# Optimization experiments

Hardware: AMD Instinct MI355X
Metric: run time of the kernel (lower is better)

## Reference

```python
import jax, jax.numpy as jnp
import numpy as np

DIM = 256
HEADS = 8
HD = DIM // HEADS        # head_dim = 32
WS = 8                   # window_size (Wh = Ww = 8)
NEXP = 8                 # num_experts
HID = 128                # attr_hidden_size (router hidden)
SCALE = HD ** -0.5


def _window_partition(x, ws):
    # (B, H, W, C) -> (B * H//ws * W//ws, ws, ws, C)
    B, H, W, C = x.shape
    x = x.reshape(B, H // ws, ws, W // ws, ws, C)
    return x.transpose(0, 1, 3, 2, 4, 5).reshape(-1, ws, ws, C)


def _window_reverse(w, ws, B, H, W):
    # inverse of _window_partition
    C = w.shape[-1]
    x = w.reshape(B, H // ws, W // ws, ws, ws, C)
    return x.transpose(0, 1, 3, 2, 4, 5).reshape(B, H, W, C)


def _rope2(x):
    # 2D rotary embedding over a window: x (B*, Wh, Ww, d).
    # First d/2 channels rotated by row position, last d/2 by column position.
    B, Wh, Ww, d = x.shape
    d2 = d // 2

    def angles(L, dd):
        inv = 1.0 / (10000.0 ** (jnp.arange(0, dd, 2, dtype=jnp.float32) / dd))
        return jnp.arange(L, dtype=jnp.float32)[:, None] * inv[None, :]  # (L, dd//2)

    def rotate(v, ang, bshape):
        # v: (B, Wh, Ww, dd) pairs interleaved; ang broadcast as bshape
        p = v.reshape(*v.shape[:-1], -1, 2)
        c = jnp.cos(ang).reshape(bshape)
        s = jnp.sin(ang).reshape(bshape)
        o0 = p[..., 0] * c - p[..., 1] * s
        o1 = p[..., 0] * s + p[..., 1] * c
        return jnp.stack([o0, o1], axis=-1).reshape(v.shape)

    ah = angles(Wh, d2)  # (Wh, d2//2)
    aw = angles(Ww, d2)  # (Ww, d2//2)
    xh = rotate(x[..., :d2], ah, (1, Wh, 1, d2 // 2))
    xw = rotate(x[..., d2:], aw, (1, 1, Ww, d2 // 2))
    return jnp.concatenate([xh, xw], axis=-1)


def _moe_linear(xf, routes, w, b):
    # Top-1 dispatch: per-expert dense GEMM, masked select (jit-safe, static shapes).
    # xf: (T, in), routes: (T,) int, w: (E, out, in), b: (E, out)
    out = jnp.zeros((xf.shape[0], w.shape[1]), xf.dtype)
    for i in range(w.shape[0]):
        y = xf @ w[i].T + b[i]
        out = jnp.where((routes == i)[:, None], y, out)
    return out


def setup_inputs() -> dict:
    key = jax.random.key(0)
    ks = jax.random.split(key, 8)
    sc = 0.02
    return {
        "x": jax.random.normal(ks[0], (8, 64, 64, DIM), jnp.float32),
        "router_w1": jax.random.normal(ks[1], (HID, DIM), jnp.float32) * sc,
        "router_b1": jnp.zeros((HID,), jnp.float32),
        "router_w2": jax.random.normal(ks[2], (NEXP, HID), jnp.float32) * sc,
        "router_b2": jnp.zeros((NEXP,), jnp.float32),
        "qkv_w": jax.random.normal(ks[3], (NEXP, 3 * DIM, DIM), jnp.float32) * sc,
        "qkv_b": jnp.zeros((NEXP, 3 * DIM), jnp.float32),
        "proj_w": jax.random.normal(ks[4], (NEXP, DIM, DIM), jnp.float32) * sc,
        "proj_b": jnp.zeros((NEXP, DIM), jnp.float32),
    }


def reference(x, router_w1, router_b1, router_w2, router_b2,
              qkv_w, qkv_b, proj_w, proj_b):
    Bs, H, W, C = x.shape
    xf = x.reshape(-1, C)  # (T, C), T = Bs*H*W

    # --- Top-1 router (eval mode: no noise, no token dropping) ---
    h = jax.nn.relu(xf @ router_w1.T + router_b1)
    router_logits = h @ router_w2.T + router_b2          # (T, E)
    router_probs = jax.nn.softmax(router_logits, axis=-1)
    route_prob_max = jnp.max(router_probs, axis=-1)       # (T,)
    routes = jnp.argmax(router_probs, axis=-1)            # (T,)

    # --- per-expert QKV projection (grouped dispatch) ---
    qkv = _moe_linear(xf, routes, qkv_w, qkv_b)           # (T, 3C)
    qkv = qkv.reshape(Bs, H, W, 3 * C)

    # --- window partition (shift=0, dilated=1 -> no roll, mask=None) ---
    qw = _window_partition(qkv, WS).reshape(-1, WS * WS, 3 * C)
    B_, N, _ = qw.shape
    qkv5 = qw.reshape(B_, N, 3, HEADS, HD).transpose(2, 0, 3, 1, 4)  # (3,B_,h,N,hd)
    q, k, v = qkv5[0], qkv5[1], qkv5[2]

    # --- RoPE on q, k over the 2D window ---
    q = _rope2(q.reshape(-1, WS, WS, HD)).reshape(B_, HEADS, N, HD)
    k = _rope2(k.reshape(-1, WS, WS, HD)).reshape(B_, HEADS, N, HD)

    # --- windowed attention (moe_mask is all zeros in eval: no drops) ---
    attn = jax.nn.softmax((q * SCALE) @ k.swapaxes(-2, -1), axis=-1)  # (B_,h,N,N)
    out = (attn @ v).swapaxes(1, 2).reshape(B_, N, C)

    # --- window reverse ---
    out = _window_reverse(out.reshape(-1, WS, WS, C), WS, Bs, H, W)

    # --- per-expert output projection + Switch-style prob scaling ---
    of = _moe_linear(out.reshape(-1, C), routes, proj_w, proj_b)
    of = of * route_prob_max[:, None]
    return of.reshape(Bs, H, W, C)
```

## Files before the change

### kernel.cpp

```cpp
#include <hip/hip_runtime.h>
#include <hip/hip_bf16.h>

typedef unsigned short u16;
typedef unsigned int u32;
typedef __attribute__((ext_vector_type(8))) short short8;
typedef __attribute__((ext_vector_type(4))) float f32x4;

#define T_TOK 32768
#define SCALE_ATT 0.17677669529663687f

__device__ __forceinline__ u16 f2bf(float f){
  u32 u = __float_as_uint(f);
  u32 r = u + 0x7fffu + ((u >> 16) & 1u);
  return (u16)(r >> 16);
}
__device__ __forceinline__ float bf2f(u16 h){
  return __uint_as_float(((u32)h) << 16);
}

__device__ __forceinline__ int xcd_swz(int flat, int nwg){
  return (flat & 7) * (nwg >> 3) + (flat >> 3);
}

__global__ __launch_bounds__(256) void k_prep(
    const float* __restrict__ qkvw, u16* __restrict__ qw_bf,
    const float* __restrict__ projw, u16* __restrict__ pw_bf,
    const float* __restrict__ rw1, u16* __restrict__ w1h, u16* __restrict__ w1l,
    int* __restrict__ sorted, int* __restrict__ counts, int* __restrict__ cursors)
{
  int b = blockIdx.x, tid = threadIdx.x;
  if (b < 1536){
    int i = b * 256 + tid;
    float4 v = ((const float4*)qkvw)[i];
    ushort4 o;
    o.x = f2bf(v.x); o.y = f2bf(v.y); o.z = f2bf(v.z); o.w = f2bf(v.w);
    ((ushort4*)qw_bf)[i] = o;
  } else if (b < 2048){
    int i = (b - 1536) * 256 + tid;
    float4 v = ((const float4*)projw)[i];
    ushort4 o;
    o.x = f2bf(v.x); o.y = f2bf(v.y); o.z = f2bf(v.z); o.w = f2bf(v.w);
    ((ushort4*)pw_bf)[i] = o;
  } else if (b < 2176){
    int i = (b - 2048) * 256 + tid;
    float v = rw1[i];
    u16 h = f2bf(v);
    w1h[i] = h;
    w1l[i] = f2bf(v - bf2f(h));
  } else if (b < 2209){
    int i = (b - 2176) * 256 + tid;
    int4 m1 = {-1, -1, -1, -1};
    ((int4*)sorted)[i] = m1;
  } else {
    if (tid < 8){ counts[tid] = 0; cursors[tid] = 0; }
  }
}

__global__ __launch_bounds__(256) void k_router(
    const float* __restrict__ x, const u16* __restrict__ w1h, const u16* __restrict__ w1l,
    const float* __restrict__ b1, const float* __restrict__ w2, const float* __restrict__ b2,
    int* __restrict__ routes, float* __restrict__ pmax, int* __restrict__ counts,
    u16* __restrict__ x_bf)
{
  __shared__ __align__(16) char smem[64*132*4];
  u16* Ah = (u16*)smem;
  u16* Al = Ah + 2560;
  u16* Bh = Al + 2560;
  u16* Bl = Bh + 5120;
  float* Hs = (float*)smem;
  __shared__ int lhist[8];

  int tid = threadIdx.x;
  int t0 = blockIdx.x * 64;
  int wv = tid >> 6, lane = tid & 63, quad = lane >> 4, l16 = lane & 15;
  if (tid < 8) lhist[tid] = 0;

  int arow = tid >> 2, acg = tid & 3;
  int brow = tid >> 1, bhalf = tid & 1;

  f32x4 acc[4][2];
  #pragma unroll
  for (int i = 0; i < 4; ++i)
    #pragma unroll
    for (int j = 0; j < 2; ++j)
      #pragma unroll
      for (int rr = 0; rr < 4; ++rr) acc[i][j][rr] = 0.f;

  for (int kt = 0; kt < 8; ++kt){
    const float* gx = x + (size_t)(t0 + arow) * 256 + kt * 32 + acg * 8;
    float4 v0 = *(const float4*)gx;
    float4 v1 = *(const float4*)(gx + 4);
    ushort4 h0, h1, l0, l1;
    h0.x = f2bf(v0.x); h0.y = f2bf(v0.y); h0.z = f2bf(v0.z); h0.w = f2bf(v0.w);
    h1.x = f2bf(v1.x); h1.y = f2bf(v1.y); h1.z = f2bf(v1.z); h1.w = f2bf(v1.w);
    l0.x = f2bf(v0.x - bf2f(h0.x)); l0.y = f2bf(v0.y - bf2f(h0.y));
    l0.z = f2bf(v0.z - bf2f(h0.z)); l0.w = f2bf(v0.w - bf2f(h0.w));
    l1.x = f2bf(v1.x - bf2f(h1.x)); l1.y = f2bf(v1.y - bf2f(h1.y));
    l1.z = f2bf(v1.z - bf2f(h1.z)); l1.w = f2bf(v1.w - bf2f(h1.w));
    u16* gxb = x_bf + (size_t)(t0 + arow) * 256 + kt * 32 + acg * 8;
    *(ushort4*)gxb = h0; *(ushort4*)(gxb + 4) = h1;
    const u16* gwh = w1h + (size_t)brow * 256 + kt * 32 + bhalf * 16;
    const u16* gwl = w1l + (size_t)brow * 256 + kt * 32 + bhalf * 16;
    uint4 wh0 = *(const uint4*)gwh;
    uint4 wh1 = *(const uint4*)(gwh + 8);
    uint4 wl0 = *(const uint4*)gwl;
    uint4 wl1 = *(const uint4*)(gwl + 8);
    __syncthreads();
    *(ushort4*)&Ah[arow*40 + acg*8    ] = h0;
    *(ushort4*)&Ah[arow*40 + acg*8 + 4] = h1;
    *(ushort4*)&Al[arow*40 + acg*8    ] = l0;
    *(ushort4*)&Al[arow*40 + acg*8 + 4] = l1;
    *(uint4*)&Bh[brow*40 + bhalf*16    ] = wh0;
    *(uint4*)&Bh[brow*40 + bhalf*16 + 8] = wh1;
    *(uint4*)&Bl[brow*40 + bhalf*16    ] = wl0;
    *(uint4*)&Bl[brow*40 + bhalf*16 + 8] = wl1;
    __syncthreads();
    short8 ah[4], al[4], bhf[2], blf[2];
    #pragma unroll
    for (int i = 0; i < 4; ++i){
      ah[i] = *(const short8*)&Ah[(i*16 + l16)*40 + quad*8];
      al[i] = *(const short8*)&Al[(i*16 + l16)*40 + quad*8];
    }
    #pragma unroll
    for (int j = 0; j < 2; ++j){
      bhf[j] = *(const short8*)&Bh[(wv*32 + j*16 + l16)*40 + quad*8];
      blf[j] = *(const short8*)&Bl[(wv*32 + j*16 + l16)*40 + quad*8];
    }
    #pragma unroll
    for (int i = 0; i < 4; ++i)
      #pragma unroll
      for (int j = 0; j < 2; ++j){
        acc[i][j] = __builtin_amdgcn_mfma_f32_16x16x32_bf16(ah[i], bhf[j], acc[i][j], 0, 0, 0);
        acc[i][j] = __builtin_amdgcn_mfma_f32_16x16x32_bf16(ah[i], blf[j], acc[i][j], 0, 0, 0);
        acc[i][j] = __builtin_amdgcn_mfma_f32_16x16x32_bf16(al[i], bhf[j], acc[i][j], 0, 0, 0);
      }
  }
  __syncthreads();

  #pragma unroll
  for (int i = 0; i < 4; ++i)
    #pragma unroll
    for (int j = 0; j < 2; ++j){
      int col = wv*32 + j*16 + l16;
      float bb = b1[col];
      #pragma unroll
      for (int rr = 0; rr < 4; ++rr){
        float h = acc[i][j][rr] + bb;
        Hs[(i*16 + quad*4 + rr)*132 + col] = h > 0.f ? h : 0.f;
      }
    }
  __syncthreads();

  #pragma unroll
  for (int pass = 0; pass < 2; ++pass){
    int mtok = (tid >> 3) + pass * 32;
    int e = tid & 7;
    const float4* w2r = (const float4*)(w2 + e * 128);
    float l = b2[e];
    #pragma unroll
    for (int k4 = 0; k4 < 32; ++k4){
      float4 w = w2r[k4];
      int k = k4 * 4;
      l = fmaf(Hs[mtok*132+k  ], w.x, l);
      l = fmaf(Hs[mtok*132+k+1], w.y, l);
      l = fmaf(Hs[mtok*132+k+2], w.z, l);
      l = fmaf(Hs[mtok*132+k+3], w.w, l);
    }
    float mv = l; int mi = e;
    #pragma unroll
    for (int off = 1; off < 8; off <<= 1){
      float ov = __shfl_xor(mv, off, 64);
      int   oi = __shfl_xor(mi, off, 64);
      if (ov > mv || (ov == mv && oi < mi)){ mv = ov; mi = oi; }
    }
    float sum = expf(l - mv);
    #pragma unroll
    for (int off = 1; off < 8; off <<= 1) sum += __shfl_xor(sum, off, 64);
    if (e == 0){
      int t = t0 + mtok;
      routes[t] = mi;
      pmax[t] = 1.0f / sum;
      atomicAdd(&lhist[mi], 1);
    }
  }
  __syncthreads();
  if (tid < 8 && lhist[tid] > 0) atomicAdd(&counts[tid], lhist[tid]);
}

__global__ __launch_bounds__(256) void k_scatter(
    const int* __restrict__ routes, const int* __restrict__ counts,
    int* __restrict__ cursors, int* __restrict__ sorted, int* __restrict__ rank,
    int* __restrict__ offs)
{
  __shared__ int lc[8], lb[8], so[9];
  int tid = threadIdx.x;
  if (tid == 0){
    int o = 0; so[0] = 0;
    #pragma unroll
    for (int e = 0; e < 8; ++e){ o += ((counts[e] + 127) >> 7) << 7; so[e+1] = o; }
  }
  if (tid < 8) lc[tid] = 0;
  __syncthreads();
  int t = blockIdx.x * 256 + tid;
  int e = routes[t];
  int rl = atomicAdd(&lc[e], 1);
  __syncthreads();
  if (tid < 8 && lc[tid] > 0) lb[tid] = atomicAdd(&cursors[tid], lc[tid]);
  __syncthreads();
  int pos = so[e] + lb[e] + rl;
  sorted[pos] = t;
  rank[t] = pos;
  if (blockIdx.x == 0 && tid < 9) offs[tid] = so[tid];
}

#define ASTR 56
template<int NOUT, bool PROJ, int NB, int NWG>
__global__ __launch_bounds__(256) void k_gemm(
    const u16* __restrict__ A, const u16* __restrict__ W,
    const float* __restrict__ bias, const int* __restrict__ sidx,
    const int* __restrict__ offs, const float* __restrict__ pmax,
    u16* __restrict__ outb, float* __restrict__ outf)
{
  __shared__ __align__(16) u16 As[128 * ASTR];
  __shared__ __align__(16) u16 Bs[128 * ASTR];
  int tid = threadIdx.x;
  int flat = blockIdx.y * NB + blockIdx.x;
  int logical = xcd_swz(flat, NWG);
  int m0 = (logical / NB) * 128;
  int n0 = (logical % NB) * 128;
  int total = offs[8];
  if (m0 >= total) return;
  int e = 0;
  #pragma unroll
  for (int i = 1; i < 8; ++i) if (m0 >= offs[i]) e = i;

  int wv = tid >> 6, lane = tid & 63, quad = lane >> 4, l16 = lane & 15;
  int wrow = (wv >> 1) * 64, wcol = (wv & 1) * 64;

  int row0 = tid >> 2, c0 = tid & 3;
  const u16 *aptr0, *aptr1;
  if (PROJ){
    aptr0 = A + (size_t)(m0 + row0) * 256 + c0 * 8;
    aptr1 = aptr0 + (size_t)64 * 256;
  } else {
    int tA0 = sidx[m0 + row0];      if (tA0 < 0) tA0 = 0;
    int tA1 = sidx[m0 + row0 + 64]; if (tA1 < 0) tA1 = 0;
    aptr0 = A + (size_t)tA0 * 256 + c0 * 8;
    aptr1 = A + (size_t)tA1 * 256 + c0 * 8;
  }
  int pc = (row0 >> 4) + (row0 & 15) * 4;
  const u16* bptr0 = W + ((size_t)e * NOUT + n0 + pc) * 256 + c0 * 8;
  const u16* bptr1 = W + ((size_t)e * NOUT + n0 + 64 + pc) * 256 + c0 * 8;

  f32x4 acc[4][4];
  #pragma unroll
  for (int i = 0; i < 4; ++i)
    #pragma unroll
    for (int j = 0; j < 4; ++j)
      #pragma unroll
      for (int r = 0; r < 4; ++r) acc[i][j][r] = 0.f;

  uint4 a0 = *(const uint4*)aptr0, a1 = *(const uint4*)aptr1;
  uint4 b0 = *(const uint4*)bptr0, b1 = *(const uint4*)bptr1;

  for (int kt = 0; kt < 8; ++kt){
    __syncthreads();
    *(uint4*)&As[ row0      *ASTR + c0*8] = a0;
    *(uint4*)&As[(row0 + 64)*ASTR + c0*8] = a1;
    *(uint4*)&Bs[ row0      *ASTR + c0*8] = b0;
    *(uint4*)&Bs[(row0 + 64)*ASTR + c0*8] = b1;
    __syncthreads();
    if (kt < 7){
      a0 = *(const uint4*)(aptr0 + (kt+1)*32);
      a1 = *(const uint4*)(aptr1 + (kt+1)*32);
      b0 = *(const uint4*)(bptr0 + (kt+1)*32);
      b1 = *(const uint4*)(bptr1 + (kt+1)*32);
    }
    short8 af[4], bfv[4];
    #pragma unroll
    for (int i = 0; i < 4; ++i)
      af[i] = *(const short8*)&As[(wrow + i*16 + l16)*ASTR + quad*8];
    #pragma unroll
    for (int j = 0; j < 4; ++j)
      bfv[j] = *(const short8*)&Bs[(wcol + j*16 + l16)*ASTR + quad*8];
    #pragma unroll
    for (int i = 0; i < 4; ++i)
      #pragma unroll
      for (int j = 0; j < 4; ++j)
        acc[i][j] = __builtin_amdgcn_mfma_f32_16x16x32_bf16(af[i], bfv[j], acc[i][j], 0, 0, 0);
  }

  float4 bj4 = *(const float4*)&bias[e*NOUT + n0 + wcol + l16*4];
  if (PROJ){
    #pragma unroll
    for (int i = 0; i < 4; ++i){
      #pragma unroll
      for (int ri = 0; ri < 4; ++ri){
        int row = wrow + i*16 + quad*4 + ri;
        int t = sidx[m0 + row];
        if (t < 0) continue;
        float pm = pmax[t];
        float4 ov;
        ov.x = (acc[i][0][ri] + bj4.x) * pm;
        ov.y = (acc[i][1][ri] + bj4.y) * pm;
        ov.z = (acc[i][2][ri] + bj4.z) * pm;
        ov.w = (acc[i][3][ri] + bj4.w) * pm;
        *(float4*)&outf[(size_t)t * NOUT + n0 + wcol + l16*4] = ov;
      }
    }
  } else {
    int col0 = n0 + wcol + l16*4;
    bool isqk = (col0 < 512);
    float inv0 = 0.f, inv1 = 0.f;
    float qsc = (col0 < 256) ? SCALE_ATT : 1.0f;
    if (isqk){
      int p0 = (col0 & 15) >> 1;
      inv0 = __expf(-1.1512925465f * (float)p0);
      inv1 = inv0 * 0.31622776601683794f;
    }
    int sel  = col0 >> 8;
    int head = (col0 >> 5) & 7;
    int ch   = col0 & 31;
    size_t hb = ((size_t)(sel * 8 + head) * 512) * 2048 + ch;
    #pragma unroll
    for (int i = 0; i < 4; ++i){
      #pragma unroll
      for (int ri = 0; ri < 4; ++ri){
        int row = wrow + i*16 + quad*4 + ri;
        int t = sidx[m0 + row];
        if (t < 0) continue;
        float vx = acc[i][0][ri] + bj4.x;
        float vy = acc[i][1][ri] + bj4.y;
        float vz = acc[i][2][ri] + bj4.z;
        float vw = acc[i][3][ri] + bj4.w;
        if (isqk){
          float pos = (float)((col0 & 16) ? (t & 7) : ((t >> 6) & 7));
          float a0r = pos * inv0, a1r = pos * inv1;
          float s0, c0s, s1, c1s;
          __sincosf(a0r, &s0, &c0s);
          __sincosf(a1r, &s1, &c1s);
          float r0 = (vx*c0s - vy*s0) * qsc;
          float r1 = (vx*s0 + vy*c0s) * qsc;
          float r2 = (vz*c1s - vw*s1) * qsc;
          float r3 = (vz*s1 + vw*c1s) * qsc;
          vx = r0; vy = r1; vz = r2; vw = r3;
        }
        int win = (t >> 12) * 64 + ((t >> 9) & 7) * 8 + ((t >> 3) & 7);
        int n   = ((t >> 6) & 7) * 8 + (t & 7);
        uint2 ov;
        ov.x = (u32)f2bf(vx) | ((u32)f2bf(vy) << 16);
        ov.y = (u32)f2bf(vz) | ((u32)f2bf(vw) << 16);
        *(uint2*)&outb[hb + (size_t)win * 2048 + n * 32] = ov;
      }
    }
  }
}

__global__ __launch_bounds__(64, 3) void k_attn(const u16* __restrict__ qkv,
                                                const int* __restrict__ rank,
                                                u16* __restrict__ attn_s)
{
  __shared__ __align__(16) u16 Ps[64*72];
  __shared__ __align__(16) u16 Vt[32*72];

  int lane = threadIdx.x;
  int quad = lane >> 4, l16 = lane & 15;
  int wh = xcd_swz(blockIdx.x, 4096);
  int head = wh >> 9, win = wh & 511;
  int b = win >> 6, wy = (win >> 3) & 7, wx = win & 7;
  int tb = b*4096 + wy*512 + wx*8;

  const u16* qbase = qkv + (size_t)(head * 512 + win) * 2048;
  const u16* kbase = qbase + (size_t)8 * 512 * 2048;
  const u16* vbase = qbase + (size_t)16 * 512 * 2048;

  int rk[4][4];
  #pragma unroll
  for (int i = 0; i < 4; ++i)
    #pragma unroll
    for (int rr = 0; rr < 4; ++rr){
      int m = i*16 + quad*4 + rr;
      rk[i][rr] = rank[tb + (m >> 3) * 64 + (m & 7)];
    }

  short8 qf[4], kf[4];
  #pragma unroll
  for (int i = 0; i < 4; ++i){
    qf[i] = *(const short8*)(qbase + (i*16 + l16)*32 + quad*8);
    kf[i] = *(const short8*)(kbase + (i*16 + l16)*32 + quad*8);
  }
  uint4 va[4];
  #pragma unroll
  for (int h = 0; h < 4; ++h)
    va[h] = *(const uint4*)(vbase + h*512 + l16*32 + quad*8);

  f32x4 sa[4][4];
  #pragma unroll
  for (int i = 0; i < 4; ++i)
    #pragma unroll
    for (int j = 0; j < 4; ++j){
      #pragma unroll
      for (int rr = 0; rr < 4; ++rr) sa[i][j][rr] = 0.f;
      sa[i][j] = __builtin_amdgcn_mfma_f32_16x16x32_bf16(qf[i], kf[j], sa[i][j], 0, 0, 0);
    }

  f32x4 rs[4];
  #pragma unroll
  for (int i = 0; i < 4; ++i)
    #pragma unroll
    for (int rr = 0; rr < 4; ++rr){
      float e0 = __expf(sa[i][0][rr]);
      float e1 = __expf(sa[i][1][rr]);
      float e2 = __expf(sa[i][2][rr]);
      float e3 = __expf(sa[i][3][rr]);
      rs[i][rr] = (e0 + e1) + (e2 + e3);
      uint2 pk;
      pk.x = (u32)f2bf(e0) | ((u32)f2bf(e1) << 16);
      pk.y = (u32)f2bf(e2) | ((u32)f2bf(e3) << 16);
      *(uint2*)&Ps[(i*16 + quad*4 + rr)*72 + l16*4] = pk;
    }
  #pragma unroll
  for (int i = 0; i < 4; ++i)
    #pragma unroll
    for (int rr = 0; rr < 4; ++rr){
      #pragma unroll
      for (int off = 1; off < 16; off <<= 1)
        rs[i][rr] += __shfl_xor(rs[i][rr], off, 64);
    }

  u32* vu = (u32*)va;
  #pragma unroll
  for (int h = 0; h < 4; ++h){
    int pn = l16 * 4 + h;
    #pragma unroll
    for (int w = 0; w < 4; ++w){
      u32 vv = vu[h*4 + w];
      Vt[(quad*8 + 2*w    )*72 + pn] = (u16)(vv & 0xffff);
      Vt[(quad*8 + 2*w + 1)*72 + pn] = (u16)(vv >> 16);
    }
  }

  f32x4 oa[4][2];
  #pragma unroll
  for (int i = 0; i < 4; ++i)
    #pragma unroll
    for (int rr = 0; rr < 4; ++rr){ oa[i][0][rr] = 0.f; oa[i][1][rr] = 0.f; }
  #pragma unroll
  for (int ks = 0; ks < 2; ++ks){
    short8 vf0 = *(const short8*)&Vt[(     l16)*72 + ks*32 + quad*8];
    short8 vf1 = *(const short8*)&Vt[(16 + l16)*72 + ks*32 + quad*8];
    #pragma unroll
    for (int i = 0; i < 4; ++i){
      short8 pf = *(const short8*)&Ps[(i*16 + l16)*72 + ks*32 + quad*8];
      oa[i][0] = __builtin_amdgcn_mfma_f32_16x16x32_bf16(pf, vf0, oa[i][0], 0, 0, 0);
      oa[i][1] = __builtin_amdgcn_mfma_f32_16x16x32_bf16(pf, vf1, oa[i][1], 0, 0, 0);
    }
  }

  #pragma unroll
  for (int i = 0; i < 4; ++i)
    #pragma unroll
    for (int rr = 0; rr < 4; ++rr){
      float inv = __builtin_amdgcn_rcpf(rs[i][rr]);
      int pos = rk[i][rr];
      u16* op = attn_s + (size_t)pos * 256 + head * 32 + l16;
      op[0]  = f2bf(oa[i][0][rr] * inv);
      op[16] = f2bf(oa[i][1][rr] * inv);
    }
}

extern "C" void kernel_launch(void* const* d_in, const int* in_sizes, int n_in,
                              void* d_out, int out_size, void* d_ws, size_t ws_size,
                              hipStream_t stream){
  const float* x     = (const float*)d_in[0];
  const float* rw1   = (const float*)d_in[1];
  const float* rb1   = (const float*)d_in[2];
  const float* rw2   = (const float*)d_in[3];
  const float* rb2   = (const float*)d_in[4];
  const float* qkvw  = (const float*)d_in[5];
  const float* qkvb  = (const float*)d_in[6];
  const float* projw = (const float*)d_in[7];
  const float* projb = (const float*)d_in[8];
  float* out = (float*)d_out;

  char* ws = (char*)d_ws;
  u16*   x_bf    = (u16*)(ws);
  u16*   qkv_bf  = (u16*)(ws + 16777216);
  u16*   w1h     = (u16*)(ws + 67108864);
  u16*   w1l     = w1h + 32768;
  u16*   attn_s  = (u16*)(ws + 67108864);
  u16*   qw_bf   = (u16*)(ws + 84410368);
  u16*   pw_bf   = (u16*)(ws + 87556096);
  int*   routes  = (int*)(ws + 88604672);
  float* pmaxp   = (float*)(ws + 88735744);
  int*   sorted  = (int*)(ws + 88866816);
  int*   rank    = (int*)(ws + 89001984);
  int*   counts  = (int*)(ws + 89133056);
  int*   cursors = (int*)(ws + 89133056 + 32);
  int*   offs    = (int*)(ws + 89133056 + 64);

  k_prep<<<2210, 256, 0, stream>>>(qkvw, qw_bf, projw, pw_bf, rw1, w1h, w1l,
                                   sorted, counts, cursors);
  k_router<<<512, 256, 0, stream>>>(x, w1h, w1l, rb1, rw2, rb2, routes, pmaxp, counts, x_bf);
  k_scatter<<<128, 256, 0, stream>>>(routes, counts, cursors, sorted, rank, offs);
  k_gemm<768, false, 6, 1584><<<dim3(6, 264), 256, 0, stream>>>(
      x_bf, qw_bf, qkvb, sorted, offs, nullptr, qkv_bf, nullptr);
  k_attn<<<4096, 64, 0, stream>>>(qkv_bf, rank, attn_s);
  k_gemm<256, true, 2, 528><<<dim3(2, 264), 256, 0, stream>>>(
      attn_s, pw_bf, projb, sorted, offs, pmaxp, nullptr, out);
}
```

Baseline: 196.0 us.

## Fold weight prep into router, double-buffer GEMM tiles via direct global-to-LDS loads

```diff
diff --git a/kernel.cpp b/kernel.cpp
--- a/kernel.cpp
+++ b/kernel.cpp
@@ -22,47 +22,41 @@
   return (flat & 7) * (nwg >> 3) + (flat >> 3);
 }
 
-__global__ __launch_bounds__(256) void k_prep(
-    const float* __restrict__ qkvw, u16* __restrict__ qw_bf,
-    const float* __restrict__ projw, u16* __restrict__ pw_bf,
-    const float* __restrict__ rw1, u16* __restrict__ w1h, u16* __restrict__ w1l,
-    int* __restrict__ sorted, int* __restrict__ counts, int* __restrict__ cursors)
-{
-  int b = blockIdx.x, tid = threadIdx.x;
-  if (b < 1536){
-    int i = b * 256 + tid;
-    float4 v = ((const float4*)qkvw)[i];
-    ushort4 o;
-    o.x = f2bf(v.x); o.y = f2bf(v.y); o.z = f2bf(v.z); o.w = f2bf(v.w);
-    ((ushort4*)qw_bf)[i] = o;
-  } else if (b < 2048){
-    int i = (b - 1536) * 256 + tid;
-    float4 v = ((const float4*)projw)[i];
-    ushort4 o;
-    o.x = f2bf(v.x); o.y = f2bf(v.y); o.z = f2bf(v.z); o.w = f2bf(v.w);
-    ((ushort4*)pw_bf)[i] = o;
-  } else if (b < 2176){
-    int i = (b - 2048) * 256 + tid;
-    float v = rw1[i];
-    u16 h = f2bf(v);
-    w1h[i] = h;
-    w1l[i] = f2bf(v - bf2f(h));
-  } else if (b < 2209){
-    int i = (b - 2176) * 256 + tid;
-    int4 m1 = {-1, -1, -1, -1};
-    ((int4*)sorted)[i] = m1;
-  } else {
-    if (tid < 8){ counts[tid] = 0; cursors[tid] = 0; }
-  }
+__device__ __forceinline__ void gl16(const u16* g, u16* l){
+  __builtin_amdgcn_global_load_lds(
+      (const __attribute__((address_space(1))) u32*)g,
+      (__attribute__((address_space(3))) u32*)l, 16, 0, 0);
 }
 
 __global__ __launch_bounds__(256) void k_router(
-    const float* __restrict__ x, const u16* __restrict__ w1h, const u16* __restrict__ w1l,
+    const float* __restrict__ x, const float* __restrict__ rw1,
     const float* __restrict__ b1, const float* __restrict__ w2, const float* __restrict__ b2,
     int* __restrict__ routes, float* __restrict__ pmax, int* __restrict__ counts,
-    u16* __restrict__ x_bf)
+    u16* __restrict__ x_bf,
+    const float* __restrict__ qkvw, u16* __restrict__ qw_bf,
+    const float* __restrict__ projw, u16* __restrict__ pw_bf)
 {
   __shared__ __align__(16) char smem[64*132*4];
+  int tid = threadIdx.x;
+
+  if (blockIdx.x >= 512){
+    int b = blockIdx.x - 512;
+    if (b < 1536){
+      int i = b * 256 + tid;
+      float4 v = ((const float4*)qkvw)[i];
+      ushort4 o;
+      o.x = f2bf(v.x); o.y = f2bf(v.y); o.z = f2bf(v.z); o.w = f2bf(v.w);
+      ((ushort4*)qw_bf)[i] = o;
+    } else {
+      int i = (b - 1536) * 256 + tid;
+      float4 v = ((const float4*)projw)[i];
+      ushort4 o;
+      o.x = f2bf(v.x); o.y = f2bf(v.y); o.z = f2bf(v.z); o.w = f2bf(v.w);
+      ((ushort4*)pw_bf)[i] = o;
+    }
+    return;
+  }
+
   u16* Ah = (u16*)smem;
   u16* Al = Ah + 2560;
   u16* Bh = Al + 2560;
@@ -70,7 +64,6 @@
   float* Hs = (float*)smem;
   __shared__ int lhist[8];
 
-  int tid = threadIdx.x;
   int t0 = blockIdx.x * 64;
   int wv = tid >> 6, lane = tid & 63, quad = lane >> 4, l16 = lane & 15;
   if (tid < 8) lhist[tid] = 0;
@@ -99,21 +92,25 @@
     l1.z = f2bf(v1.z - bf2f(h1.z)); l1.w = f2bf(v1.w - bf2f(h1.w));
     u16* gxb = x_bf + (size_t)(t0 + arow) * 256 + kt * 32 + acg * 8;
     *(ushort4*)gxb = h0; *(ushort4*)(gxb + 4) = h1;
-    const u16* gwh = w1h + (size_t)brow * 256 + kt * 32 + bhalf * 16;
-    const u16* gwl = w1l + (size_t)brow * 256 + kt * 32 + bhalf * 16;
-    uint4 wh0 = *(const uint4*)gwh;
-    uint4 wh1 = *(const uint4*)(gwh + 8);
-    uint4 wl0 = *(const uint4*)gwl;
-    uint4 wl1 = *(const uint4*)(gwl + 8);
+    const float* gw = rw1 + (size_t)brow * 256 + kt * 32 + bhalf * 16;
+    ushort4 wh[4], wl[4];
+    #pragma unroll
+    for (int q = 0; q < 4; ++q){
+      float4 wf = *(const float4*)(gw + q*4);
+      wh[q].x = f2bf(wf.x); wh[q].y = f2bf(wf.y); wh[q].z = f2bf(wf.z); wh[q].w = f2bf(wf.w);
+      wl[q].x = f2bf(wf.x - bf2f(wh[q].x)); wl[q].y = f2bf(wf.y - bf2f(wh[q].y));
+      wl[q].z = f2bf(wf.z - bf2f(wh[q].z)); wl[q].w = f2bf(wf.w - bf2f(wh[q].w));
+    }
     __syncthreads();
     *(ushort4*)&Ah[arow*40 + acg*8    ] = h0;
     *(ushort4*)&Ah[arow*40 + acg*8 + 4] = h1;
     *(ushort4*)&Al[arow*40 + acg*8    ] = l0;
     *(ushort4*)&Al[arow*40 + acg*8 + 4] = l1;
-    *(uint4*)&Bh[brow*40 + bhalf*16    ] = wh0;
-    *(uint4*)&Bh[brow*40 + bhalf*16 + 8] = wh1;
-    *(uint4*)&Bl[brow*40 + bhalf*16    ] = wl0;
-    *(uint4*)&Bl[brow*40 + bhalf*16 + 8] = wl1;
+    #pragma unroll
+    for (int q = 0; q < 4; ++q){
+      *(ushort4*)&Bh[brow*40 + bhalf*16 + q*4] = wh[q];
+      *(ushort4*)&Bl[brow*40 + bhalf*16 + q*4] = wl[q];
+    }
     __syncthreads();
     short8 ah[4], al[4], bhf[2], blf[2];
     #pragma unroll
@@ -213,7 +210,6 @@
   if (blockIdx.x == 0 && tid < 9) offs[tid] = so[tid];
 }
 
-#define ASTR 56
 template<int NOUT, bool PROJ, int NB, int NWG>
 __global__ __launch_bounds__(256) void k_gemm(
     const u16* __restrict__ A, const u16* __restrict__ W,
@@ -221,8 +217,8 @@
     const int* __restrict__ offs, const float* __restrict__ pmax,
     u16* __restrict__ outb, float* __restrict__ outf)
 {
-  __shared__ __align__(16) u16 As[128 * ASTR];
-  __shared__ __align__(16) u16 Bs[128 * ASTR];
+  __shared__ __align__(1024) u16 As[2][4096];
+  __shared__ __align__(1024) u16 Bs[2][4096];
   int tid = threadIdx.x;
   int flat = blockIdx.y * NB + blockIdx.x;
   int logical = xcd_swz(flat, NWG);
@@ -237,20 +233,21 @@
   int wv = tid >> 6, lane = tid & 63, quad = lane >> 4, l16 = lane & 15;
   int wrow = (wv >> 1) * 64, wcol = (wv & 1) * 64;
 
-  int row0 = tid >> 2, c0 = tid & 3;
-  const u16 *aptr0, *aptr1;
+  int srow = wv*16 + (lane >> 2);
+  int cg = (lane & 3) ^ ((srow >> 1) & 3);
+  const u16 *ag0, *ag1;
   if (PROJ){
-    aptr0 = A + (size_t)(m0 + row0) * 256 + c0 * 8;
-    aptr1 = aptr0 + (size_t)64 * 256;
+    ag0 = A + (size_t)(m0 + srow) * 256 + cg * 8;
+    ag1 = A + (size_t)(m0 + srow + 64) * 256 + cg * 8;
   } else {
-    int tA0 = sidx[m0 + row0];      if (tA0 < 0) tA0 = 0;
-    int tA1 = sidx[m0 + row0 + 64]; if (tA1 < 0) tA1 = 0;
-    aptr0 = A + (size_t)tA0 * 256 + c0 * 8;
-    aptr1 = A + (size_t)tA1 * 256 + c0 * 8;
-  }
-  int pc = (row0 >> 4) + (row0 & 15) * 4;
-  const u16* bptr0 = W + ((size_t)e * NOUT + n0 + pc) * 256 + c0 * 8;
-  const u16* bptr1 = W + ((size_t)e * NOUT + n0 + 64 + pc) * 256 + c0 * 8;
+    int tA0 = sidx[m0 + srow];      if (tA0 < 0) tA0 = 0;
+    int tA1 = sidx[m0 + srow + 64]; if (tA1 < 0) tA1 = 0;
+    ag0 = A + (size_t)tA0 * 256 + cg * 8;
+    ag1 = A + (size_t)tA1 * 256 + cg * 8;
+  }
+  int pc = (srow >> 4) + (srow & 15) * 4;
+  const u16* bg0 = W + ((size_t)e * NOUT + n0 + pc) * 256 + cg * 8;
+  const u16* bg1 = W + ((size_t)e * NOUT + n0 + 64 + pc) * 256 + cg * 8;
 
   f32x4 acc[4][4];
   #pragma unroll
@@ -260,29 +257,34 @@
       #pragma unroll
       for (int r = 0; r < 4; ++r) acc[i][j][r] = 0.f;
 
-  uint4 a0 = *(const uint4*)aptr0, a1 = *(const uint4*)aptr1;
-  uint4 b0 = *(const uint4*)bptr0, b1 = *(const uint4*)bptr1;
-
+  int qsw8 = (quad ^ ((l16 >> 1) & 3)) * 8;
+
+  {
+    u16* a_lo = (u16*)((char*)&As[0][0] + wv*1024);
+    u16* b_lo = (u16*)((char*)&Bs[0][0] + wv*1024);
+    gl16(ag0, a_lo);  gl16(ag1, (u16*)((char*)a_lo + 4096));
+    gl16(bg0, b_lo);  gl16(bg1, (u16*)((char*)b_lo + 4096));
+  }
+
+  #pragma unroll
   for (int kt = 0; kt < 8; ++kt){
-    __syncthreads();
-    *(uint4*)&As[ row0      *ASTR + c0*8] = a0;
-    *(uint4*)&As[(row0 + 64)*ASTR + c0*8] = a1;
-    *(uint4*)&Bs[ row0      *ASTR + c0*8] = b0;
-    *(uint4*)&Bs[(row0 + 64)*ASTR + c0*8] = b1;
+    int cur = kt & 1;
     __syncthreads();
     if (kt < 7){
-      a0 = *(const uint4*)(aptr0 + (kt+1)*32);
-      a1 = *(const uint4*)(aptr1 + (kt+1)*32);
-      b0 = *(const uint4*)(bptr0 + (kt+1)*32);
-      b1 = *(const uint4*)(bptr1 + (kt+1)*32);
+      u16* a_lo = (u16*)((char*)&As[cur^1][0] + wv*1024);
+      u16* b_lo = (u16*)((char*)&Bs[cur^1][0] + wv*1024);
+      gl16(ag0 + (kt+1)*32, a_lo);
+      gl16(ag1 + (kt+1)*32, (u16*)((char*)a_lo + 4096));
+      gl16(bg0 + (kt+1)*32, b_lo);
+      gl16(bg1 + (kt+1)*32, (u16*)((char*)b_lo + 4096));
     }
     short8 af[4], bfv[4];
     #pragma unroll
     for (int i = 0; i < 4; ++i)
-      af[i] = *(const short8*)&As[(wrow + i*16 + l16)*ASTR + quad*8];
+      af[i] = *(const short8*)&As[cur][(wrow + i*16 + l16)*32 + qsw8];
     #pragma unroll
     for (int j = 0; j < 4; ++j)
-      bfv[j] = *(const short8*)&Bs[(wcol + j*16 + l16)*ASTR + quad*8];
+      bfv[j] = *(const short8*)&Bs[cur][(wcol + j*16 + l16)*32 + qsw8];
     #pragma unroll
     for (int i = 0; i < 4; ++i)
       #pragma unroll
@@ -486,8 +488,6 @@
   char* ws = (char*)d_ws;
   u16*   x_bf    = (u16*)(ws);
   u16*   qkv_bf  = (u16*)(ws + 16777216);
-  u16*   w1h     = (u16*)(ws + 67108864);
-  u16*   w1l     = w1h + 32768;
   u16*   attn_s  = (u16*)(ws + 67108864);
   u16*   qw_bf   = (u16*)(ws + 84410368);
   u16*   pw_bf   = (u16*)(ws + 87556096);
@@ -499,9 +499,10 @@
   int*   cursors = (int*)(ws + 89133056 + 32);
   int*   offs    = (int*)(ws + 89133056 + 64);
 
-  k_prep<<<2210, 256, 0, stream>>>(qkvw, qw_bf, projw, pw_bf, rw1, w1h, w1l,
-                                   sorted, counts, cursors);
-  k_router<<<512, 256, 0, stream>>>(x, w1h, w1l, rb1, rw2, rb2, routes, pmaxp, counts, x_bf);
+  hipMemsetAsync(counts, 0, 64, stream);
+  hipMemsetAsync(sorted, 0xFF, 135168, stream);
+  k_router<<<2560, 256, 0, stream>>>(x, rw1, rb1, rw2, rb2, routes, pmaxp, counts,
+                                     x_bf, qkvw, qw_bf, projw, pw_bf);
   k_scatter<<<128, 256, 0, stream>>>(routes, counts, cursors, sorted, rank, offs);
   k_gemm<768, false, 6, 1584><<<dim3(6, 264), 256, 0, stream>>>(
       x_bf, qw_bf, qkvb, sorted, offs, nullptr, qkv_bf, nullptr);
```

Measured after the change: 199.7 us. About the same (+1.9%).
